# Kernel tuning notes

Measured on AMD Instinct MI355X. Metric: run time of the kernel, lower is better.

The kernel has to match this reference:

```python
import jax, jax.numpy as jnp
import numpy as np

N = 100000   # nodes
E = 1600000  # edges (avg degree 16)
B = 64       # graphs in batch
D_IN = 64
D = 64       # d_model


def setup_inputs() -> dict:
    key = jax.random.key(0)
    ks = jax.random.split(key, 12)
    inp = {}
    inp["x_raw"] = jax.random.normal(ks[0], (N, D_IN), dtype=jnp.float32)
    inp["edge_index"] = jax.random.randint(ks[1], (2, E), 0, N)
    inp["batch"] = jnp.sort(jax.random.randint(ks[2], (N,), 0, B))
    # SAGEConv params per layer: lin_l (weight+bias, applied to neighbor mean),
    # lin_r (weight only, applied to root) -- PyG defaults.
    dins = [D_IN, D, D]
    for i, din in enumerate(dins):
        scale = 1.0 / np.sqrt(din)
        inp[f"Wl{i}"] = jax.random.normal(ks[3 + 3 * i], (D, din), dtype=jnp.float32) * scale
        inp[f"bl{i}"] = jnp.zeros((D,), dtype=jnp.float32)
        inp[f"Wr{i}"] = jax.random.normal(ks[4 + 3 * i], (D, din), dtype=jnp.float32) * scale
    return inp


def _sage_conv(x, src, dst, Wl, bl, Wr):
    """PyG SAGEConv(normalize=True): mean-aggregate neighbors, lin_l + lin_r, L2 norm."""
    msg = jax.ops.segment_sum(x[src], dst, num_segments=N)          # [N, d_in]
    deg = jax.ops.segment_sum(jnp.ones((src.shape[0],), x.dtype), dst, num_segments=N)
    mean = msg / jnp.maximum(deg, 1.0)[:, None]
    out = mean @ Wl.T + bl + x @ Wr.T                               # [N, D]
    nrm = jnp.sqrt(jnp.sum(out * out, axis=-1, keepdims=True))
    return out / jnp.maximum(nrm, 1e-12)


def reference(x_raw, edge_index, batch, Wl0, bl0, Wr0, Wl1, bl1, Wr1, Wl2, bl2, Wr2):
    src, dst = edge_index[0], edge_index[1]
    # dropout is identity in eval mode
    h = jax.nn.relu(_sage_conv(x_raw, src, dst, Wl0, bl0, Wr0))
    h = jax.nn.relu(_sage_conv(h, src, dst, Wl1, bl1, Wr1))
    h = jax.nn.relu(_sage_conv(h, src, dst, Wl2, bl2, Wr2))
    # readout='sum': scatter-sum over batch ids -> [B, D]
    return jax.ops.segment_sum(h, batch, num_segments=B)
```

## Files before the change

### kernel.cpp

```cpp
#include <hip/hip_runtime.h>

#define DFEAT 64

typedef __attribute__((ext_vector_type(8))) short bf16x8;
typedef __attribute__((ext_vector_type(4))) float f32x4;

__device__ __forceinline__ float bfhi(unsigned int u) {
    return __builtin_bit_cast(float, u & 0xFFFF0000u);
}
__device__ __forceinline__ float bflo(unsigned int u) {
    return __builtin_bit_cast(float, u << 16);
}
__device__ __forceinline__ unsigned short f2bf(float f) {
    unsigned int u = __builtin_bit_cast(unsigned int, f);
    u += 0x7FFFu + ((u >> 16) & 1u);
    return (unsigned short)(u >> 16);
}

__global__ void __launch_bounds__(256)
cvt_bf16_kernel(const float* __restrict__ in, unsigned short* __restrict__ outb,
                int n4) {
    int i = blockIdx.x * 256 + threadIdx.x;
    if (i >= n4) return;
    const float4 v = reinterpret_cast<const float4*>(in)[i];
    uint2 p;
    p.x = (unsigned int)f2bf(v.x) | ((unsigned int)f2bf(v.y) << 16);
    p.y = (unsigned int)f2bf(v.z) | ((unsigned int)f2bf(v.w) << 16);
    reinterpret_cast<uint2*>(outb)[i] = p;
}


__global__ void __launch_bounds__(256)
bucket_hist_kernel(const int* __restrict__ dsts, int* __restrict__ bhist, int E) {
    __shared__ int h[512];
    const int tid = threadIdx.x;
    h[tid] = 0; h[tid + 256] = 0;
    __syncthreads();
    for (int e = blockIdx.x * 256 + tid; e < E; e += gridDim.x * 256)
        atomicAdd(&h[dsts[e] >> 8], 1);
    __syncthreads();
    for (int b = tid; b < 512; b += 256)
        if (h[b]) atomicAdd(&bhist[b], h[b]);
}

__global__ void __launch_bounds__(256)
bucket_scan_kernel(const int* __restrict__ bhist, int* __restrict__ bbase,
                   int* __restrict__ bcur) {
    __shared__ int sm[512];
    const int tid = threadIdx.x;
    sm[tid] = bhist[tid]; sm[tid + 256] = bhist[tid + 256];
    __syncthreads();
    for (int s = 1; s < 512; s <<= 1) {
        int a0 = (tid >= s) ? sm[tid - s] : 0;
        int a1 = sm[tid + 256 - s];
        __syncthreads();
        sm[tid] += a0; sm[tid + 256] += a1;
        __syncthreads();
    }
    for (int b = tid; b < 512; b += 256) {
        int excl = b ? sm[b - 1] : 0;
        bbase[b] = excl; bcur[b] = excl;
    }
    if (tid == 0) bbase[512] = sm[511];
}

#define BIN_CH 2048
__global__ void __launch_bounds__(256)
bin_kernel(const int* __restrict__ srcs, const int* __restrict__ dsts,
           int* __restrict__ bcur, unsigned int* __restrict__ pairbuf, int E) {
    __shared__ int hist[512];
    __shared__ int sscan[512];
    __shared__ int gbase[512];
    __shared__ unsigned int staged[BIN_CH];
    __shared__ unsigned short sbkt[BIN_CH];

    const int tid = threadIdx.x;
    const int base = blockIdx.x * BIN_CH;
    const int chcnt = min(BIN_CH, E - base);

    hist[tid] = 0; hist[tid + 256] = 0;
    __syncthreads();

    unsigned int pk[8];
    unsigned short bb[8], rr[8];
#pragma unroll
    for (int k = 0; k < 8; ++k) {
        int i = k * 256 + tid;
        if (i < chcnt) {
            int e = base + i;
            int d = dsts[e];
            int s = srcs[e];
            int b = d >> 8;
            int r = atomicAdd(&hist[b], 1);
            pk[k] = ((unsigned int)(d & 255) << 24) | (unsigned int)s;
            bb[k] = (unsigned short)b;
            rr[k] = (unsigned short)r;
        } else {
            bb[k] = 0xFFFFu;
        }
    }
    __syncthreads();

    sscan[tid] = hist[tid]; sscan[tid + 256] = hist[tid + 256];
    __syncthreads();
    for (int s = 1; s < 512; s <<= 1) {
        int a0 = (tid >= s) ? sscan[tid - s] : 0;
        int a1 = sscan[tid + 256 - s];
        __syncthreads();
        sscan[tid] += a0; sscan[tid + 256] += a1;
        __syncthreads();
    }

    for (int b = tid; b < 512; b += 256) {
        int c = hist[b];
        gbase[b] = c ? atomicAdd(&bcur[b], c) : 0;
    }
    __syncthreads();

#pragma unroll
    for (int k = 0; k < 8; ++k) {
        if (bb[k] != 0xFFFFu) {
            int b = bb[k];
            int lpos = (b ? sscan[b - 1] : 0) + rr[k];
            staged[lpos] = pk[k];
            sbkt[lpos] = (unsigned short)b;
        }
    }
    __syncthreads();

    for (int i = tid; i < chcnt; i += 256) {
        int b = sbkt[i];
        int excl = b ? sscan[b - 1] : 0;
        pairbuf[gbase[b] + (i - excl)] = staged[i];
    }
}

__global__ void __launch_bounds__(256)
bucket_fill_kernel(const unsigned int* __restrict__ pairbuf,
                   const int* __restrict__ bbase,
                   int* __restrict__ rowptr, int* __restrict__ col,
                   int N, int E) {
    __shared__ int hist[256];
    __shared__ int scan_[256];
    __shared__ int cur[256];

    const int tid = threadIdx.x;
    const int b = blockIdx.x;
    const int node0 = b << 8;
    const int bb0 = bbase[b];
    const int cnt = bbase[b + 1] - bb0;

    hist[tid] = 0;
    __syncthreads();
    for (int i = tid; i < cnt; i += 256)
        atomicAdd(&hist[pairbuf[bb0 + i] >> 24], 1);
    __syncthreads();

    scan_[tid] = hist[tid];
    __syncthreads();
    for (int s = 1; s < 256; s <<= 1) {
        int a = (tid >= s) ? scan_[tid - s] : 0;
        __syncthreads();
        scan_[tid] += a;
        __syncthreads();
    }
    int excl = tid ? scan_[tid - 1] : 0;
    if (node0 + tid < N) rowptr[node0 + tid] = bb0 + excl;
    if (b == 0 && tid == 0) rowptr[N] = E;
    cur[tid] = bb0 + excl;
    __syncthreads();

    for (int i = tid; i < cnt; i += 256) {
        unsigned int p = pairbuf[bb0 + i];
        int pos = atomicAdd(&cur[p >> 24], 1);
        col[pos] = (int)(p & 0xFFFFFFu);
    }
}

__global__ void __launch_bounds__(256, 4)
fused_sage_kernel(const unsigned short* __restrict__ xb,
                  const int* __restrict__ rowptr, const int* __restrict__ col,
                  const float* __restrict__ Wl, const float* __restrict__ bl,
                  const float* __restrict__ Wr,
                  unsigned short* __restrict__ h_out,
                  const int* __restrict__ batch, float* __restrict__ out,
                  int n_nodes, int final_layer) {
    __shared__ __align__(16) unsigned short Wlds[8192];

    const int tid = threadIdx.x;

    for (int i4 = tid; i4 < 1024; i4 += 256) {
        const float4 wl = reinterpret_cast<const float4*>(Wl)[i4];
        const float4 wr = reinterpret_cast<const float4*>(Wr)[i4];
        const int feat = i4 >> 4;
        const int n = feat >> 4, cc = feat & 15;
        const int k0 = (i4 & 15) << 2;
        const int qq = (k0 >> 3) & 3, tl = k0 >> 5, j0 = k0 & 7;
        const int lofs = (qq * 16 + cc) * 8 + j0;
        unsigned short* d0 = &Wlds[(n * 4 + tl) * 512 + lofs];
        d0[0] = f2bf(wl.x); d0[1] = f2bf(wl.y); d0[2] = f2bf(wl.z); d0[3] = f2bf(wl.w);
        unsigned short* d1 = &Wlds[(n * 4 + 2 + tl) * 512 + lofs];
        d1[0] = f2bf(wr.x); d1[1] = f2bf(wr.y); d1[2] = f2bf(wr.z); d1[3] = f2bf(wr.w);
    }
    __syncthreads();

    const int tiles = (n_nodes + 15) >> 4;
    const int tile = blockIdx.x * 4 + (tid >> 6);
    if (tile >= tiles) return;

    const int lane = tid & 63;
    const int c = lane & 15;
    const int q = lane >> 4;
    const bf16x8* fragp = reinterpret_cast<const bf16x8*>(Wlds);

    const int base = tile << 4;
    const bool valid = (base + c) < n_nodes;
    const int node = valid ? (base + c) : (n_nodes - 1);

    const uint4* rows4 = reinterpret_cast<const uint4*>(xb);
    const int st = rowptr[node];
    const int deg = valid ? (rowptr[node + 1] - st) : 0;

    float accA[8], accB[8];
#pragma unroll
    for (int j = 0; j < 8; ++j) { accA[j] = 0.f; accB[j] = 0.f; }

    if (deg > 0) {
        int nbB = col[st];
        uint4 a0 = rows4[(size_t)nbB * 8 + q];
        uint4 b0 = rows4[(size_t)nbB * 8 + 4 + q];
        nbB = col[st + min(1, deg - 1)];
        for (int j = 0; j < deg; ++j) {
            const int nbC = col[st + min(j + 2, deg - 1)];
            const uint4 a1 = rows4[(size_t)nbB * 8 + q];
            const uint4 b1 = rows4[(size_t)nbB * 8 + 4 + q];
            accA[0] += bflo(a0.x); accA[1] += bfhi(a0.x);
            accA[2] += bflo(a0.y); accA[3] += bfhi(a0.y);
            accA[4] += bflo(a0.z); accA[5] += bfhi(a0.z);
            accA[6] += bflo(a0.w); accA[7] += bfhi(a0.w);
            accB[0] += bflo(b0.x); accB[1] += bfhi(b0.x);
            accB[2] += bflo(b0.y); accB[3] += bfhi(b0.y);
            accB[4] += bflo(b0.z); accB[5] += bfhi(b0.z);
            accB[6] += bflo(b0.w); accB[7] += bfhi(b0.w);
            a0 = a1; b0 = b1; nbB = nbC;
        }
    }

    const float inv = (deg > 0) ? (1.0f / (float)deg) : 0.0f;
    bf16x8 F0, F1;
#pragma unroll
    for (int j = 0; j < 8; ++j) {
        F0[j] = (short)f2bf(accA[j] * inv);
        F1[j] = (short)f2bf(accB[j] * inv);
    }
    const uint4* xrow = reinterpret_cast<const uint4*>(&xb[(size_t)node * 64]);
    const bf16x8 F2 = __builtin_bit_cast(bf16x8, xrow[q]);
    const bf16x8 F3 = __builtin_bit_cast(bf16x8, xrow[4 + q]);

    f32x4 acc[4];
#pragma unroll
    for (int n = 0; n < 4; ++n) acc[n] = (f32x4){0.f, 0.f, 0.f, 0.f};

#pragma unroll
    for (int n = 0; n < 4; ++n) {
        bf16x8 w0 = fragp[(n * 4 + 0) * 64 + lane];
        bf16x8 w1 = fragp[(n * 4 + 1) * 64 + lane];
        bf16x8 w2 = fragp[(n * 4 + 2) * 64 + lane];
        bf16x8 w3 = fragp[(n * 4 + 3) * 64 + lane];
        acc[n] = __builtin_amdgcn_mfma_f32_16x16x32_bf16(w0, F0, acc[n], 0, 0, 0);
        acc[n] = __builtin_amdgcn_mfma_f32_16x16x32_bf16(w1, F1, acc[n], 0, 0, 0);
        acc[n] = __builtin_amdgcn_mfma_f32_16x16x32_bf16(w2, F2, acc[n], 0, 0, 0);
        acc[n] = __builtin_amdgcn_mfma_f32_16x16x32_bf16(w3, F3, acc[n], 0, 0, 0);
    }

    float v[4][4];
    float ss = 0.f;
#pragma unroll
    for (int n = 0; n < 4; ++n) {
        const float4 b4 = reinterpret_cast<const float4*>(bl)[n * 4 + q];
        v[n][0] = acc[n][0] + b4.x;
        v[n][1] = acc[n][1] + b4.y;
        v[n][2] = acc[n][2] + b4.z;
        v[n][3] = acc[n][3] + b4.w;
#pragma unroll
        for (int r = 0; r < 4; ++r) ss += v[n][r] * v[n][r];
    }
    ss += __shfl_xor(ss, 16, 64);
    ss += __shfl_xor(ss, 32, 64);
    const float nrm = 1.0f / fmaxf(sqrtf(ss), 1e-12f);

    if (!final_layer) {
        if (valid) {
            uint2* dst = reinterpret_cast<uint2*>(&h_out[(size_t)(base + c) * 64]);
#pragma unroll
            for (int n = 0; n < 4; ++n) {
                float o0 = fmaxf(v[n][0] * nrm, 0.f), o1 = fmaxf(v[n][1] * nrm, 0.f);
                float o2 = fmaxf(v[n][2] * nrm, 0.f), o3 = fmaxf(v[n][3] * nrm, 0.f);
                uint2 p;
                p.x = (unsigned int)f2bf(o0) | ((unsigned int)f2bf(o1) << 16);
                p.y = (unsigned int)f2bf(o2) | ((unsigned int)f2bf(o3) << 16);
                dst[n * 4 + q] = p;
            }
        }
    } else {
        float o[4][4];
#pragma unroll
        for (int n = 0; n < 4; ++n)
#pragma unroll
            for (int r = 0; r < 4; ++r)
                o[n][r] = valid ? fmaxf(v[n][r] * nrm, 0.f) : 0.f;

        const int lastn = min(base + 15, n_nodes - 1);
        const int gb0 = batch[base];
        if (gb0 == batch[lastn]) {
#pragma unroll
            for (int n = 0; n < 4; ++n)
#pragma unroll
                for (int r = 0; r < 4; ++r) {
                    float s = o[n][r];
                    s += __shfl_xor(s, 1, 64);
                    s += __shfl_xor(s, 2, 64);
                    s += __shfl_xor(s, 4, 64);
                    s += __shfl_xor(s, 8, 64);
                    if (c == 0)
                        atomicAdd(&out[(size_t)gb0 * DFEAT + n * 16 + q * 4 + r], s);
                }
        } else {
            if (valid) {
                const int gb = batch[base + c];
#pragma unroll
                for (int n = 0; n < 4; ++n)
#pragma unroll
                    for (int r = 0; r < 4; ++r)
                        atomicAdd(&out[(size_t)gb * DFEAT + n * 16 + q * 4 + r], o[n][r]);
            }
        }
    }
}

extern "C" void kernel_launch(void* const* d_in, const int* in_sizes, int n_in,
                              void* d_out, int out_size, void* d_ws, size_t ws_size,
                              hipStream_t stream) {
    const float* x_raw = (const float*)d_in[0];
    const int*   eidx  = (const int*)d_in[1];
    const int*   batch = (const int*)d_in[2];
    const float* Wl0 = (const float*)d_in[3];
    const float* bl0 = (const float*)d_in[4];
    const float* Wr0 = (const float*)d_in[5];
    const float* Wl1 = (const float*)d_in[6];
    const float* bl1 = (const float*)d_in[7];
    const float* Wr1 = (const float*)d_in[8];
    const float* Wl2 = (const float*)d_in[9];
    const float* bl2 = (const float*)d_in[10];
    const float* Wr2 = (const float*)d_in[11];

    const int N = in_sizes[0] / DFEAT;
    const int E = in_sizes[1] / 2;
    const int* srcs = eidx;
    const int* dsts = eidx + E;
    float* out = (float*)d_out;

    const int NB = (N + 255) >> 8;

    char* ws = (char*)d_ws;
    auto align512 = [](size_t v) { return (v + 511) & ~(size_t)511; };
    size_t off = 0;
    int* rowptr = (int*)(ws + off); off += align512(((size_t)N + 1) * 4);
    int* col    = (int*)(ws + off); off += align512((size_t)E * 4);
    int* bhist  = (int*)(ws + off); off += align512(512 * 4);
    int* bbase  = (int*)(ws + off); off += align512(513 * 4);
    int* bcur   = (int*)(ws + off); off += align512(512 * 4);
    unsigned short* xb = (unsigned short*)(ws + off); off += align512((size_t)N * DFEAT * 2);
    unsigned short* hA = (unsigned short*)(ws + off); off += align512((size_t)N * DFEAT * 2);
    unsigned short* hB = (unsigned short*)(ws + off);
    unsigned int* pairbuf = (unsigned int*)hA;

    hipMemsetAsync(bhist, 0, 512 * 4, stream);
    hipMemsetAsync(out, 0, (size_t)out_size * 4, stream);

    const int n4 = N * DFEAT / 4;
    cvt_bf16_kernel<<<(n4 + 255) / 256, 256, 0, stream>>>(x_raw, xb, n4);

    bucket_hist_kernel<<<512, 256, 0, stream>>>(dsts, bhist, E);
    bucket_scan_kernel<<<1, 256, 0, stream>>>(bhist, bbase, bcur);
    bin_kernel<<<(E + BIN_CH - 1) / BIN_CH, 256, 0, stream>>>(srcs, dsts, bcur, pairbuf, E);
    bucket_fill_kernel<<<NB, 256, 0, stream>>>(pairbuf, bbase, rowptr, col, N, E);

    const int tiles    = (N + 15) / 16;
    const int xfBlocks = (tiles + 3) / 4;

    fused_sage_kernel<<<xfBlocks, 256, 0, stream>>>(xb, rowptr, col, Wl0, bl0, Wr0,
                                                    hA, nullptr, nullptr, N, 0);
    fused_sage_kernel<<<xfBlocks, 256, 0, stream>>>(hA, rowptr, col, Wl1, bl1, Wr1,
                                                    hB, nullptr, nullptr, N, 0);
    fused_sage_kernel<<<xfBlocks, 256, 0, stream>>>(hB, rowptr, col, Wl2, bl2, Wr2,
                                                    nullptr, batch, out, N, 1);
}
```

Measured before the change: 315.3 us.

## Split neighbor aggregation of each 16-node tile across four wavefronts

Each block now handles one 16-node tile instead of four. Its four wavefronts stride over each node's neighbor list and combine their partial sums through LDS float atomics, and wavefront 0 then runs the MFMA projection and normalization. The goal is more memory-level parallelism on the latency-bound gather per node. The cost is four times as many blocks, so the weight matrices are converted into LDS four times as often, plus the LDS atomics, an extra barrier, and three wavefronts idle during the epilogue. The weight LDS stores are also packed into 64-bit writes.

```diff
diff --git a/kernel.cpp b/kernel.cpp
--- a/kernel.cpp
+++ b/kernel.cpp
@@ -186,9 +186,11 @@
                   const int* __restrict__ batch, float* __restrict__ out,
                   int n_nodes, int final_layer) {
     __shared__ __align__(16) unsigned short Wlds[8192];
+    __shared__ float accL[16 * 64];
 
     const int tid = threadIdx.x;
 
+    for (int i = tid; i < 1024; i += 256) accL[i] = 0.f;
     for (int i4 = tid; i4 < 1024; i4 += 256) {
         const float4 wl = reinterpret_cast<const float4*>(Wl)[i4];
         const float4 wr = reinterpret_cast<const float4*>(Wr)[i4];
@@ -197,23 +199,22 @@
         const int k0 = (i4 & 15) << 2;
         const int qq = (k0 >> 3) & 3, tl = k0 >> 5, j0 = k0 & 7;
         const int lofs = (qq * 16 + cc) * 8 + j0;
-        unsigned short* d0 = &Wlds[(n * 4 + tl) * 512 + lofs];
-        d0[0] = f2bf(wl.x); d0[1] = f2bf(wl.y); d0[2] = f2bf(wl.z); d0[3] = f2bf(wl.w);
-        unsigned short* d1 = &Wlds[(n * 4 + 2 + tl) * 512 + lofs];
-        d1[0] = f2bf(wr.x); d1[1] = f2bf(wr.y); d1[2] = f2bf(wr.z); d1[3] = f2bf(wr.w);
-    }
-    __syncthreads();
-
-    const int tiles = (n_nodes + 15) >> 4;
-    const int tile = blockIdx.x * 4 + (tid >> 6);
-    if (tile >= tiles) return;
-
+        uint2 pl, pr;
+        pl.x = (unsigned int)f2bf(wl.x) | ((unsigned int)f2bf(wl.y) << 16);
+        pl.y = (unsigned int)f2bf(wl.z) | ((unsigned int)f2bf(wl.w) << 16);
+        pr.x = (unsigned int)f2bf(wr.x) | ((unsigned int)f2bf(wr.y) << 16);
+        pr.y = (unsigned int)f2bf(wr.z) | ((unsigned int)f2bf(wr.w) << 16);
+        *reinterpret_cast<uint2*>(&Wlds[(n * 4 + tl) * 512 + lofs]) = pl;
+        *reinterpret_cast<uint2*>(&Wlds[(n * 4 + 2 + tl) * 512 + lofs]) = pr;
+    }
+    __syncthreads();
+
+    const int w = tid >> 6;
     const int lane = tid & 63;
     const int c = lane & 15;
     const int q = lane >> 4;
-    const bf16x8* fragp = reinterpret_cast<const bf16x8*>(Wlds);
-
-    const int base = tile << 4;
+
+    const int base = blockIdx.x << 4;
     const bool valid = (base + c) < n_nodes;
     const int node = valid ? (base + c) : (n_nodes - 1);
 
@@ -225,15 +226,17 @@
 #pragma unroll
     for (int j = 0; j < 8; ++j) { accA[j] = 0.f; accB[j] = 0.f; }
 
-    if (deg > 0) {
-        int nbB = col[st];
-        uint4 a0 = rows4[(size_t)nbB * 8 + q];
-        uint4 b0 = rows4[(size_t)nbB * 8 + 4 + q];
-        nbB = col[st + min(1, deg - 1)];
-        for (int j = 0; j < deg; ++j) {
-            const int nbC = col[st + min(j + 2, deg - 1)];
-            const uint4 a1 = rows4[(size_t)nbB * 8 + q];
-            const uint4 b1 = rows4[(size_t)nbB * 8 + 4 + q];
+    if (deg > w) {
+        const int dm1 = deg - 1;
+        const int* cp = col + st;
+        int c0 = cp[w];
+        uint4 a0 = rows4[(size_t)c0 * 8 + q];
+        uint4 b0 = rows4[(size_t)c0 * 8 + 4 + q];
+        int c1 = cp[min(w + 4, dm1)];
+        for (int j = w; j < deg; j += 4) {
+            const int c2 = cp[min(j + 8, dm1)];
+            const uint4 a1 = rows4[(size_t)c1 * 8 + q];
+            const uint4 b1 = rows4[(size_t)c1 * 8 + 4 + q];
             accA[0] += bflo(a0.x); accA[1] += bfhi(a0.x);
             accA[2] += bflo(a0.y); accA[3] += bfhi(a0.y);
             accA[4] += bflo(a0.z); accA[5] += bfhi(a0.z);
@@ -242,21 +245,30 @@
             accB[2] += bflo(b0.y); accB[3] += bfhi(b0.y);
             accB[4] += bflo(b0.z); accB[5] += bfhi(b0.z);
             accB[6] += bflo(b0.w); accB[7] += bfhi(b0.w);
-            a0 = a1; b0 = b1; nbB = nbC;
-        }
-    }
+            a0 = a1; b0 = b1; c1 = c2;
+        }
+#pragma unroll
+        for (int j = 0; j < 8; ++j) {
+            atomicAdd(&accL[j * 64 + lane], accA[j]);
+            atomicAdd(&accL[(8 + j) * 64 + lane], accB[j]);
+        }
+    }
+    __syncthreads();
+
+    if (w != 0) return;
 
     const float inv = (deg > 0) ? (1.0f / (float)deg) : 0.0f;
     bf16x8 F0, F1;
 #pragma unroll
     for (int j = 0; j < 8; ++j) {
-        F0[j] = (short)f2bf(accA[j] * inv);
-        F1[j] = (short)f2bf(accB[j] * inv);
+        F0[j] = (short)f2bf(accL[j * 64 + lane] * inv);
+        F1[j] = (short)f2bf(accL[(8 + j) * 64 + lane] * inv);
     }
     const uint4* xrow = reinterpret_cast<const uint4*>(&xb[(size_t)node * 64]);
     const bf16x8 F2 = __builtin_bit_cast(bf16x8, xrow[q]);
     const bf16x8 F3 = __builtin_bit_cast(bf16x8, xrow[4 + q]);
 
+    const bf16x8* fragp = reinterpret_cast<const bf16x8*>(Wlds);
     f32x4 acc[4];
 #pragma unroll
     for (int n = 0; n < 4; ++n) acc[n] = (f32x4){0.f, 0.f, 0.f, 0.f};
@@ -386,13 +398,12 @@
     bin_kernel<<<(E + BIN_CH - 1) / BIN_CH, 256, 0, stream>>>(srcs, dsts, bcur, pairbuf, E);
     bucket_fill_kernel<<<NB, 256, 0, stream>>>(pairbuf, bbase, rowptr, col, N, E);
 
-    const int tiles    = (N + 15) / 16;
-    const int xfBlocks = (tiles + 3) / 4;
-
-    fused_sage_kernel<<<xfBlocks, 256, 0, stream>>>(xb, rowptr, col, Wl0, bl0, Wr0,
-                                                    hA, nullptr, nullptr, N, 0);
-    fused_sage_kernel<<<xfBlocks, 256, 0, stream>>>(hA, rowptr, col, Wl1, bl1, Wr1,
-                                                    hB, nullptr, nullptr, N, 0);
-    fused_sage_kernel<<<xfBlocks, 256, 0, stream>>>(hB, rowptr, col, Wl2, bl2, Wr2,
-                                                    nullptr, batch, out, N, 1);
-}
+    const int tiles = (N + 15) / 16;
+
+    fused_sage_kernel<<<tiles, 256, 0, stream>>>(xb, rowptr, col, Wl0, bl0, Wr0,
+                                                 hA, nullptr, nullptr, N, 0);
+    fused_sage_kernel<<<tiles, 256, 0, stream>>>(hA, rowptr, col, Wl1, bl1, Wr1,
+                                                 hB, nullptr, nullptr, N, 0);
+    fused_sage_kernel<<<tiles, 256, 0, stream>>>(hB, rowptr, col, Wl2, bl2, Wr2,
+                                                 nullptr, batch, out, N, 1);
+}
```

Measured after the change: 699.3 us. 122% more time.
